# Optimization experiments

Measured on AMD Instinct MI355X. Metric: run time of the kernel, lower is better.

## Reference

```python
import jax, jax.numpy as jnp
import numpy as np

EMBED = 64
NHEADS = 8
DK = EMBED // NHEADS          # 8
PS = 32                       # patchsize[log2(8)] = (32, 32) for every head


def lrelu(z):
    return jnp.where(z > 0, z, 0.2 * z)


def conv1x1(x, w, b):
    # x: [B,C,H,W], w: [O,C], b: [O]
    return jnp.einsum('oc,bchw->bohw', w, x) + b[None, :, None, None]


def conv3x3_reflect(x, w, b, dilation=1):
    p = dilation  # pad == dilation keeps spatial size for k=3
    xp = jnp.pad(x, ((0, 0), (0, 0), (p, p), (p, p)), mode='reflect')
    y = jax.lax.conv_general_dilated(
        xp, w, window_strides=(1, 1), padding='VALID',
        rhs_dilation=(dilation, dilation),
        dimension_numbers=('NCHW', 'OIHW', 'NCHW'))
    return y + b[None, :, None, None]


def setup_inputs() -> dict:
    key = jax.random.key(0)
    ks = jax.random.split(key, 16)
    B, C, H, W = 8, EMBED, 256, 256
    g = 0.02
    inp = {
        'x': jax.random.normal(ks[0], (B, C, H, W), jnp.float32),
        'm': jax.random.uniform(ks[1], (B, 1, H, W), jnp.float32),
        'wq': jax.random.normal(ks[2], (C, C), jnp.float32) * g,
        'bq': jnp.zeros((C,), jnp.float32),
        'wk': jax.random.normal(ks[3], (C, C), jnp.float32) * g,
        'bk': jnp.zeros((C,), jnp.float32),
        'wv': jax.random.normal(ks[4], (C, C), jnp.float32) * g,
        'bv': jnp.zeros((C,), jnp.float32),
        'wo': jax.random.normal(ks[5], (C, C, 3, 3), jnp.float32) * g,
        'bo': jnp.zeros((C,), jnp.float32),
        'wf1': jax.random.normal(ks[6], (C, C, 3, 3), jnp.float32) * g,
        'bf1': jnp.zeros((C,), jnp.float32),
        'wf2': jax.random.normal(ks[7], (C, C, 3, 3), jnp.float32) * g,
        'bf2': jnp.zeros((C,), jnp.float32),
    }
    return inp


def _window(t, b, oh, ow):
    # [B, C, H, W] -> [B, nH, oh*ow, dk*ps*ps] (head = channel chunk)
    t = t.reshape(b, NHEADS, DK, oh, PS, ow, PS)
    t = t.transpose(0, 1, 3, 5, 2, 4, 6)
    return t.reshape(b, NHEADS, oh * ow, DK * PS * PS)


def _forward(x, m, wq, bq, wk, bk, wv, bv, wo, bo, wf1, bf1, wf2, bf2):
    b, c, h, w = x.shape
    oh, ow = h // PS, w // PS
    q = _window(conv1x1(x, wq, bq), b, oh, ow)
    k = _window(conv1x1(x, wk, bk), b, oh, ow)
    v = _window(conv1x1(x, wv, bv), b, oh, ow)
    # NOTE: original code calls scores.masked_fill(mm, -1e9) non-in-place and
    # discards the result, so the mask `m` does NOT affect the math. Faithful.
    scale = 1.0 / jnp.sqrt(jnp.asarray(DK * PS * PS, x.dtype))
    scores = jnp.einsum('bhqe,bhke->bhqk', q, k) * scale  # [B,nH,oh*ow,oh*ow]
    p = jax.nn.softmax(scores, axis=-1)
    y = jnp.einsum('bhqk,bhke->bhqe', p, v)
    # un-window back to [B, C, H, W] (head order == channel-chunk order)
    y = y.reshape(b, NHEADS, oh, ow, DK, PS, PS)
    y = y.transpose(0, 1, 4, 2, 5, 3, 6).reshape(b, c, h, w)
    x1 = x + lrelu(conv3x3_reflect(y, wo, bo))
    ff = lrelu(conv3x3_reflect(x1, wf1, bf1, dilation=2))
    ff = lrelu(conv3x3_reflect(ff, wf2, bf2, dilation=1))
    return x1 + ff


def reference(x, m, wq, bq, wk, bk, wv, bv, wo, bo, wf1, bf1, wf2, bf2):
    return _forward(x, m, wq, bq, wk, bk, wv, bv, wo, bo, wf1, bf1, wf2, bf2)
```

## Files before the change

kernel.cpp:

```cpp
#include <hip/hip_runtime.h>
#include <hip/hip_fp16.h>

#define SCALE 0.011048543456039806f

typedef _Float16 half8 __attribute__((ext_vector_type(8)));
typedef float f32x4 __attribute__((ext_vector_type(4)));
typedef unsigned int uint32;

__device__ inline float ldval(const float* p, int i)  { return p[i]; }
__device__ inline float ldval(const __half* p, int i) { return __half2float(p[i]); }
__device__ inline void  stval(float* p, int i, float v)  { p[i] = v; }
__device__ inline void  stval(__half* p, int i, float v) { p[i] = __float2half(v); }

__global__ __launch_bounds__(256) void prep_kernel(const float* __restrict__ wq,
                                                   const float* __restrict__ wk,
                                                   const float* __restrict__ wv,
                                                   const float* __restrict__ wo,
                                                   const float* __restrict__ wf1,
                                                   const float* __restrict__ wf2,
                                                   float* __restrict__ scr) {
    int i = blockIdx.x * 256 + threadIdx.x;
    if (i < 262144) { scr[i] = 0.f; return; }
    __half* wh = (__half*)(scr + 262144);
    int j = i - 262144;
    if (j < 12288) {
        int gm = j >> 6, c = j & 63;
        int mtx = gm >> 6, o = gm & 63;
        const float* src = (mtx == 0) ? wq : ((mtx == 1) ? wk : wv);
        wh[j] = __float2half(src[o * 64 + c]);
    } else {
        int r = j - 12288;
        int mtx = r / 36864;
        int q2 = r - mtx * 36864;
        int tap = q2 >> 12;
        int oc = q2 & 4095;
        int o = oc >> 6, c = oc & 63;
        const float* src = (mtx == 0) ? wo : ((mtx == 1) ? wf1 : wf2);
        wh[j] = __float2half(src[(o * 64 + c) * 9 + tap]);
    }
}

__global__ __launch_bounds__(512) void qkv_mfma(const float* __restrict__ x,
                                                const __half* __restrict__ wqkv,
                                                const float* __restrict__ bq,
                                                const float* __restrict__ bk,
                                                const float* __restrict__ bv,
                                                __half* __restrict__ q,
                                                __half* __restrict__ k,
                                                __half* __restrict__ v) {
    __shared__ __align__(16) __half Xs[256 * 72];
    __shared__ __align__(16) __half Ws[192 * 72];
    int t = threadIdx.x;
    int bx = blockIdx.x;
    int b = bx >> 8, row = bx & 255;
    int hw0 = row << 8;
    int bbase = b << 22;

    for (int i = 0; i < 32; i++) {
        int idx = i * 512 + t;
        int c = idx >> 8, p = idx & 255;
        Xs[p * 72 + c] = __float2half(x[bbase + (c << 16) + hw0 + p]);
    }
    const uint32* src = (const uint32*)wqkv;
    #pragma unroll
    for (int i = 0; i < 12; i++) {
        int idx = i * 512 + t;
        int o = idx >> 5, c2 = idx & 31;
        *(uint32*)&Ws[o * 72 + c2 * 2] = src[idx];
    }
    __syncthreads();

    int wave = t >> 6, lane = t & 63;
    int l15 = lane & 15, quad = lane >> 4;
    int mg = wave >> 2, ng = wave & 3;
    f32x4 acc[4][6];
    #pragma unroll
    for (int i = 0; i < 4; i++)
        #pragma unroll
        for (int m = 0; m < 6; m++) acc[i][m] = (f32x4){0.f, 0.f, 0.f, 0.f};

    #pragma unroll
    for (int kc = 0; kc < 2; kc++) {
        half8 af[6];
        #pragma unroll
        for (int m = 0; m < 6; m++)
            af[m] = *(const half8*)&Ws[((mg * 6 + m) * 16 + l15) * 72 + kc * 32 + quad * 8];
        #pragma unroll
        for (int i = 0; i < 4; i++) {
            half8 bf = *(const half8*)&Xs[(ng * 64 + i * 16 + l15) * 72 + kc * 32 + quad * 8];
            #pragma unroll
            for (int m = 0; m < 6; m++)
                acc[i][m] = __builtin_amdgcn_mfma_f32_16x16x32_f16(af[m], bf, acc[i][m], 0, 0, 0);
        }
    }
    #pragma unroll
    for (int i = 0; i < 4; i++) {
        int pix = hw0 + ng * 64 + i * 16 + l15;
        #pragma unroll
        for (int m = 0; m < 6; m++) {
            int gm = mg * 6 + m;
            int mtx = gm >> 2;
            int ob = (gm & 3) * 16 + quad * 4;
            __half* dst = (mtx == 0) ? q : ((mtx == 1) ? k : v);
            const float* bb = (mtx == 0) ? bq : ((mtx == 1) ? bk : bv);
            #pragma unroll
            for (int r = 0; r < 4; r++) {
                float z = acc[i][m][r] + bb[ob + r];
                dst[bbase + ((ob + r) << 16) + pix] = __float2half(z);
            }
        }
    }
}

__global__ __launch_bounds__(256) void scores_kernel(const __half* __restrict__ q,
                                                     const __half* __restrict__ k,
                                                     float* __restrict__ sc) {
    __shared__ float Qs[64][68];
    __shared__ float Ks[64][68];
    int ec = blockIdx.x;
    int bh = blockIdx.y;
    int b = bh >> 3, h = bh & 7;
    int cbase = ((b * 64 + h * 8 + ec) << 16);
    int t = threadIdx.x;
    int qg = t >> 4, kg = t & 15;
    float acc[4][4] = {};
    for (int j = 0; j < 16; j++) {
        __syncthreads();
        #pragma unroll
        for (int i = 0; i < 16; i++) {
            int idx = i * 256 + t;
            int wi = idx >> 6;
            int el = idx & 63;
            int eg = j * 64 + el;
            int py = eg >> 5, px = eg & 31;
            int oy = wi >> 3, ox = wi & 7;
            int a = cbase + ((oy * 32 + py) << 8) + ox * 32 + px;
            Qs[el][wi] = __half2float(q[a]);
            Ks[el][wi] = __half2float(k[a]);
        }
        __syncthreads();
        for (int e = 0; e < 64; e++) {
            float4 qv = *(const float4*)&Qs[e][qg * 4];
            float4 kv = *(const float4*)&Ks[e][kg * 4];
            float qa[4] = {qv.x, qv.y, qv.z, qv.w};
            float ka[4] = {kv.x, kv.y, kv.z, kv.w};
            #pragma unroll
            for (int i = 0; i < 4; i++)
                #pragma unroll
                for (int jj = 0; jj < 4; jj++)
                    acc[i][jj] += qa[i] * ka[jj];
        }
    }
    float* dst = sc + bh * 4096;
    #pragma unroll
    for (int i = 0; i < 4; i++)
        #pragma unroll
        for (int jj = 0; jj < 4; jj++)
            atomicAdd(&dst[(qg * 4 + i) * 64 + kg * 4 + jj], acc[i][jj]);
}

__global__ __launch_bounds__(64) void softmax_kernel(float* __restrict__ sc) {
    int row = blockIdx.x;
    int ki = threadIdx.x;
    float s = sc[row * 64 + ki] * SCALE;
    float m = s;
    #pragma unroll
    for (int off = 32; off; off >>= 1) m = fmaxf(m, __shfl_xor(m, off));
    float e = __expf(s - m);
    float sum = e;
    #pragma unroll
    for (int off = 32; off; off >>= 1) sum += __shfl_xor(sum, off);
    sc[row * 64 + ki] = e / sum;
}

__global__ __launch_bounds__(256) void attnout_kernel(const float* __restrict__ p,
                                                      const __half* __restrict__ v,
                                                      __half* __restrict__ y) {
    __shared__ float Ps[64][65];
    __shared__ float Vs[64][132];
    int dk = blockIdx.x, bh = blockIdx.y;
    int b = bh >> 3, h = bh & 7;
    int cbase = ((b * 64 + h * 8 + dk) << 16);
    int t = threadIdx.x;
    #pragma unroll
    for (int i = 0; i < 16; i++) {
        int idx = i * 256 + t;
        Ps[idx >> 6][idx & 63] = p[bh * 4096 + idx];
    }
    int qg = t >> 4, eg = t & 15;
    for (int sub = 0; sub < 8; sub++) {
        __syncthreads();
        #pragma unroll
        for (int i = 0; i < 32; i++) {
            int idx = i * 256 + t;
            int ki = idx >> 7, el = idx & 127;
            int elg = sub * 128 + el;
            int py = elg >> 5, px = elg & 31;
            int oy = ki >> 3, ox = ki & 7;
            Vs[ki][el] = __half2float(v[cbase + ((oy * 32 + py) << 8) + ox * 32 + px]);
        }
        __syncthreads();
        float acc[4][8] = {};
        for (int ki = 0; ki < 64; ki++) {
            float4 v0 = *(const float4*)&Vs[ki][eg * 8];
            float4 v1 = *(const float4*)&Vs[ki][eg * 8 + 4];
            #pragma unroll
            for (int i = 0; i < 4; i++) {
                float pv = Ps[qg * 4 + i][ki];
                acc[i][0] += pv * v0.x; acc[i][1] += pv * v0.y;
                acc[i][2] += pv * v0.z; acc[i][3] += pv * v0.w;
                acc[i][4] += pv * v1.x; acc[i][5] += pv * v1.y;
                acc[i][6] += pv * v1.z; acc[i][7] += pv * v1.w;
            }
        }
        int elg0 = sub * 128 + eg * 8;
        int py = elg0 >> 5, px = elg0 & 31;
        #pragma unroll
        for (int i = 0; i < 4; i++) {
            int wi = qg * 4 + i;
            int oy = wi >> 3, ox = wi & 7;
            int a = cbase + ((oy * 32 + py) << 8) + ox * 32 + px;
            #pragma unroll
            for (int jj = 0; jj < 8; jj++)
                y[a + jj] = __float2half(acc[i][jj]);
        }
    }
}

template <int DIL, typename TRES, typename TOUT>
__global__ __launch_bounds__(256) void conv3x3_mfma(const __half* __restrict__ in,
                                                    const __half* __restrict__ wt,
                                                    const float* __restrict__ bias,
                                                    const TRES* __restrict__ res,
                                                    TOUT* __restrict__ out) {
    constexpr int TH = 8, TW = 32;
    constexpr int PH = TH + 2 * DIL, PW = TW + 2 * DIL;
    constexpr int NP = PH * PW;
    __shared__ __align__(16) __half Xs[NP * 72];
    __shared__ __align__(16) __half Ws[64 * 72];

    int t = threadIdx.x;
    int bx = blockIdx.x;
    int tc = bx & 7, tr = (bx >> 3) & 31, b = bx >> 8;
    int x0 = tc * TW, y0 = tr * TH;
    int bbase = b << 22;

    for (int i = 0; i < NP * 64 / 256; i++) {
        int idx = i * 256 + t;
        int c = idx / NP, p = idx - c * NP;
        int py = p / PW, px = p - py * PW;
        int gy = y0 + py - DIL; gy = gy < 0 ? -gy : (gy > 255 ? 510 - gy : gy);
        int gx = x0 + px - DIL; gx = gx < 0 ? -gx : (gx > 255 ? 510 - gx : gx);
        Xs[p * 72 + c] = in[bbase + (c << 16) + (gy << 8) + gx];
    }

    int wave = t >> 6, lane = t & 63;
    int l15 = lane & 15, quad = lane >> 4;
    f32x4 acc[4][4];
    #pragma unroll
    for (int i = 0; i < 4; i++)
        #pragma unroll
        for (int m = 0; m < 4; m++) acc[i][m] = (f32x4){0.f, 0.f, 0.f, 0.f};

    for (int tap = 0; tap < 9; tap++) {
        __syncthreads();
        const uint32* src = (const uint32*)(wt + tap * 4096);
        #pragma unroll
        for (int i = 0; i < 8; i++) {
            int idx = i * 256 + t;
            int o = idx >> 5, c2 = idx & 31;
            *(uint32*)&Ws[o * 72 + c2 * 2] = src[idx];
        }
        __syncthreads();
        int ky = tap / 3, kx = tap - ky * 3;
        #pragma unroll
        for (int kc = 0; kc < 2; kc++) {
            half8 af[4];
            #pragma unroll
            for (int m = 0; m < 4; m++)
                af[m] = *(const half8*)&Ws[(m * 16 + l15) * 72 + kc * 32 + quad * 8];
            #pragma unroll
            for (int i = 0; i < 4; i++) {
                int nt = wave * 4 + i;
                int py = (nt >> 1) + ky * DIL;
                int px = (nt & 1) * 16 + l15 + kx * DIL;
                half8 bf = *(const half8*)&Xs[(py * PW + px) * 72 + kc * 32 + quad * 8];
                #pragma unroll
                for (int m = 0; m < 4; m++)
                    acc[i][m] = __builtin_amdgcn_mfma_f32_16x16x32_f16(af[m], bf, acc[i][m], 0, 0, 0);
            }
        }
    }

    #pragma unroll
    for (int i = 0; i < 4; i++) {
        int nt = wave * 4 + i;
        int hw = ((y0 + (nt >> 1)) << 8) + x0 + (nt & 1) * 16 + l15;
        #pragma unroll
        for (int m = 0; m < 4; m++) {
            #pragma unroll
            for (int r = 0; r < 4; r++) {
                int o = m * 16 + quad * 4 + r;
                float z = acc[i][m][r] + bias[o];
                z = z > 0.f ? z : 0.2f * z;
                int ga = bbase + (o << 16) + hw;
                if (res) z += ldval(res, ga);
                stval(out, ga, z);
            }
        }
    }
}

extern "C" void kernel_launch(void* const* d_in, const int* in_sizes, int n_in,
                              void* d_out, int out_size, void* d_ws, size_t ws_size,
                              hipStream_t stream) {
    const float* x   = (const float*)d_in[0];
    float*       scr = (float*)d_in[1];
    const float* wq  = (const float*)d_in[2];
    const float* bq  = (const float*)d_in[3];
    const float* wk  = (const float*)d_in[4];
    const float* bk  = (const float*)d_in[5];
    const float* wv  = (const float*)d_in[6];
    const float* bv  = (const float*)d_in[7];
    const float* wo  = (const float*)d_in[8];
    const float* bo  = (const float*)d_in[9];
    const float* wf1 = (const float*)d_in[10];
    const float* bf1 = (const float*)d_in[11];
    const float* wf2 = (const float*)d_in[12];
    const float* bf2 = (const float*)d_in[13];

    __half* wsA  = (__half*)d_ws;
    __half* wsB  = (__half*)((char*)d_ws + 67108864);
    __half* vbuf = (__half*)d_out;
    __half* ybuf = vbuf + 33554432;
    float*  outf = (float*)d_out;
    float*  sc   = scr;
    const __half* wh    = (const __half*)(scr + 262144);
    const __half* wqkv  = wh;
    const __half* wTo   = wh + 12288;
    const __half* wT1   = wh + 12288 + 36864;
    const __half* wT2   = wh + 12288 + 73728;

    prep_kernel<<<1504, 256, 0, stream>>>(wq, wk, wv, wo, wf1, wf2, scr);
    qkv_mfma<<<2048, 512, 0, stream>>>(x, wqkv, bq, bk, bv, wsA, wsB, vbuf);
    scores_kernel<<<dim3(8, 64), 256, 0, stream>>>(wsA, wsB, sc);
    softmax_kernel<<<4096, 64, 0, stream>>>(sc);
    attnout_kernel<<<dim3(8, 64), 256, 0, stream>>>(sc, vbuf, ybuf);
    conv3x3_mfma<1, float, __half><<<2048, 256, 0, stream>>>(ybuf, wTo, bo, x, wsA);
    conv3x3_mfma<2, float, __half><<<2048, 256, 0, stream>>>(wsA, wT1, bf1, (const float*)nullptr, wsB);
    conv3x3_mfma<1, __half, float><<<2048, 256, 0, stream>>>(wsB, wT2, bf2, wsA, outf);
}
```

Measured before the change: 978.1 us.

## Use NHWC intermediates, register-resident weights and swizzled LDS in 3x3 convs

Rewrites the three 3x3 conv kernels so intermediate activations between them are stored channel-last (NHWC half). Tiles can then be loaded with 16-byte vector loads instead of scalar gathers. Each wave keeps its 16 output channels' weights for all 9 taps in registers, which removes the per-tap shared-memory weight staging and 18 barriers. The input tile in LDS uses an XOR swizzle instead of padding to avoid bank conflicts. This raises register pressure (144 VGPRs for weights plus 64 accumulators), which may lower occupancy.

```diff
diff --git a/kernel.cpp b/kernel.cpp
--- a/kernel.cpp
+++ b/kernel.cpp
@@ -4,13 +4,9 @@
 #define SCALE 0.011048543456039806f
 
 typedef _Float16 half8 __attribute__((ext_vector_type(8)));
+typedef _Float16 h4    __attribute__((ext_vector_type(4)));
 typedef float f32x4 __attribute__((ext_vector_type(4)));
 typedef unsigned int uint32;
-
-__device__ inline float ldval(const float* p, int i)  { return p[i]; }
-__device__ inline float ldval(const __half* p, int i) { return __half2float(p[i]); }
-__device__ inline void  stval(float* p, int i, float v)  { p[i] = v; }
-__device__ inline void  stval(__half* p, int i, float v) { p[i] = __float2half(v); }
 
 __global__ __launch_bounds__(256) void prep_kernel(const float* __restrict__ wq,
                                                    const float* __restrict__ wk,
@@ -227,86 +223,119 @@
     }
 }
 
-template <int DIL, typename TRES, typename TOUT>
-__global__ __launch_bounds__(256) void conv3x3_mfma(const __half* __restrict__ in,
-                                                    const __half* __restrict__ wt,
-                                                    const float* __restrict__ bias,
-                                                    const TRES* __restrict__ res,
-                                                    TOUT* __restrict__ out) {
+template <int DIL, int IN_NCHW, int RES, int OUTM>
+__global__ __launch_bounds__(256) void conv3x3_v2(const _Float16* __restrict__ in,
+                                                  const _Float16* __restrict__ wt,
+                                                  const float* __restrict__ bias,
+                                                  const void* __restrict__ res,
+                                                  void* __restrict__ out) {
     constexpr int TH = 8, TW = 32;
     constexpr int PH = TH + 2 * DIL, PW = TW + 2 * DIL;
     constexpr int NP = PH * PW;
-    __shared__ __align__(16) __half Xs[NP * 72];
-    __shared__ __align__(16) __half Ws[64 * 72];
+    __shared__ __align__(16) _Float16 Xs[NP * 64];
 
     int t = threadIdx.x;
+    int wave = t >> 6, lane = t & 63;
     int bx = blockIdx.x;
     int tc = bx & 7, tr = (bx >> 3) & 31, b = bx >> 8;
     int x0 = tc * TW, y0 = tr * TH;
-    int bbase = b << 22;
-
-    for (int i = 0; i < NP * 64 / 256; i++) {
-        int idx = i * 256 + t;
-        int c = idx / NP, p = idx - c * NP;
-        int py = p / PW, px = p - py * PW;
-        int gy = y0 + py - DIL; gy = gy < 0 ? -gy : (gy > 255 ? 510 - gy : gy);
-        int gx = x0 + px - DIL; gx = gx < 0 ? -gx : (gx > 255 ? 510 - gx : gx);
-        Xs[p * 72 + c] = in[bbase + (c << 16) + (gy << 8) + gx];
-    }
-
-    int wave = t >> 6, lane = t & 63;
+    int bb = b << 22;
+
+    if (IN_NCHW) {
+        constexpr int PO = (NP + 7) / 8;
+        constexpr int SIT = (PO * 8 * 64) / 256;
+        for (int i = 0; i < SIT; i++) {
+            int s = i * 256 + t;
+            int l = s & 63, G = s >> 6;
+            int p = (G >> 3) * 8 + (l & 7);
+            int c = (G & 7) * 8 + (l >> 3);
+            int py = p / PW, px = p - py * PW;
+            int gy = y0 + py - DIL; gy = gy < 0 ? -gy : (gy > 255 ? 510 - gy : gy);
+            int gx = x0 + px - DIL; gx = gx < 0 ? -gx : (gx > 255 ? 510 - gx : gx);
+            _Float16 val = in[bb + (c << 16) + (gy << 8) + gx];
+            if (p < NP)
+                Xs[(p << 6) + (((c >> 3) ^ (p & 7)) << 3) + (c & 7)] = val;
+        }
+    } else {
+        constexpr int SLOTS = NP * 8;
+        constexpr int SIT = (SLOTS + 255) / 256;
+        half8 tmp[SIT];
+        #pragma unroll
+        for (int i = 0; i < SIT; i++) {
+            int s = i * 256 + t;
+            int p = s >> 3, c8 = s & 7;
+            int py = p / PW, px = p - py * PW;
+            int gy = y0 + py - DIL; gy = gy < 0 ? -gy : (gy > 255 ? 510 - gy : gy);
+            int gx = x0 + px - DIL; gx = gx < 0 ? -gx : (gx > 255 ? 510 - gx : gx);
+            tmp[i] = *(const half8*)(in + bb + (((gy << 8) + gx) << 6) + c8 * 8);
+        }
+        #pragma unroll
+        for (int i = 0; i < SIT; i++) {
+            int s = i * 256 + t;
+            int p = s >> 3, c8 = s & 7;
+            if (s < SLOTS)
+                *(half8*)&Xs[(p << 6) + ((c8 ^ (p & 7)) << 3)] = tmp[i];
+        }
+    }
+
     int l15 = lane & 15, quad = lane >> 4;
-    f32x4 acc[4][4];
-    #pragma unroll
-    for (int i = 0; i < 4; i++)
-        #pragma unroll
-        for (int m = 0; m < 4; m++) acc[i][m] = (f32x4){0.f, 0.f, 0.f, 0.f};
-
+    half8 af[9][2];
+    #pragma unroll
+    for (int tap = 0; tap < 9; tap++)
+        #pragma unroll
+        for (int kc = 0; kc < 2; kc++)
+            af[tap][kc] = *(const half8*)&wt[tap * 4096 + (wave * 16 + l15) * 64 + kc * 32 + quad * 8];
+
+    f32x4 acc[16];
+    #pragma unroll
+    for (int nt = 0; nt < 16; nt++) acc[nt] = (f32x4){0.f, 0.f, 0.f, 0.f};
+
+    __syncthreads();
+
+    #pragma unroll
     for (int tap = 0; tap < 9; tap++) {
-        __syncthreads();
-        const uint32* src = (const uint32*)(wt + tap * 4096);
-        #pragma unroll
-        for (int i = 0; i < 8; i++) {
-            int idx = i * 256 + t;
-            int o = idx >> 5, c2 = idx & 31;
-            *(uint32*)&Ws[o * 72 + c2 * 2] = src[idx];
-        }
-        __syncthreads();
-        int ky = tap / 3, kx = tap - ky * 3;
+        const int ky = tap / 3, kx = tap % 3;
         #pragma unroll
         for (int kc = 0; kc < 2; kc++) {
-            half8 af[4];
-            #pragma unroll
-            for (int m = 0; m < 4; m++)
-                af[m] = *(const half8*)&Ws[(m * 16 + l15) * 72 + kc * 32 + quad * 8];
-            #pragma unroll
-            for (int i = 0; i < 4; i++) {
-                int nt = wave * 4 + i;
-                int py = (nt >> 1) + ky * DIL;
-                int px = (nt & 1) * 16 + l15 + kx * DIL;
-                half8 bf = *(const half8*)&Xs[(py * PW + px) * 72 + kc * 32 + quad * 8];
-                #pragma unroll
-                for (int m = 0; m < 4; m++)
-                    acc[i][m] = __builtin_amdgcn_mfma_f32_16x16x32_f16(af[m], bf, acc[i][m], 0, 0, 0);
+            int cq = kc * 4 + quad;
+            #pragma unroll
+            for (int nt = 0; nt < 16; nt++) {
+                int p = ((nt >> 1) + ky * DIL) * PW + (nt & 1) * 16 + kx * DIL + l15;
+                half8 bf = *(const half8*)&Xs[(p << 6) + ((cq ^ (p & 7)) << 3)];
+                acc[nt] = __builtin_amdgcn_mfma_f32_16x16x32_f16(af[tap][kc], bf, acc[nt], 0, 0, 0);
             }
         }
     }
 
-    #pragma unroll
-    for (int i = 0; i < 4; i++) {
-        int nt = wave * 4 + i;
-        int hw = ((y0 + (nt >> 1)) << 8) + x0 + (nt & 1) * 16 + l15;
-        #pragma unroll
-        for (int m = 0; m < 4; m++) {
-            #pragma unroll
-            for (int r = 0; r < 4; r++) {
-                int o = m * 16 + quad * 4 + r;
-                float z = acc[i][m][r] + bias[o];
-                z = z > 0.f ? z : 0.2f * z;
-                int ga = bbase + (o << 16) + hw;
-                if (res) z += ldval(res, ga);
-                stval(out, ga, z);
-            }
+    int oc0 = wave * 16 + quad * 4;
+    f32x4 b4 = *(const f32x4*)&bias[oc0];
+    #pragma unroll
+    for (int nt = 0; nt < 16; nt++) {
+        int pixg = ((y0 + (nt >> 1)) << 8) + x0 + (nt & 1) * 16 + l15;
+        float z[4];
+        #pragma unroll
+        for (int r = 0; r < 4; r++) {
+            float w = acc[nt][r] + b4[r];
+            z[r] = w > 0.f ? w : 0.2f * w;
+        }
+        if (RES == 1) {
+            const float* rf = (const float*)res;
+            #pragma unroll
+            for (int r = 0; r < 4; r++) z[r] += rf[bb + ((oc0 + r) << 16) + pixg];
+        } else if (RES == 2) {
+            h4 rv = *(const h4*)((const _Float16*)res + bb + (pixg << 6) + oc0);
+            #pragma unroll
+            for (int r = 0; r < 4; r++) z[r] += (float)rv[r];
+        }
+        if (OUTM == 0) {
+            h4 ov;
+            #pragma unroll
+            for (int r = 0; r < 4; r++) ov[r] = (_Float16)z[r];
+            *(h4*)((_Float16*)out + bb + (pixg << 6) + oc0) = ov;
+        } else {
+            #pragma unroll
+            for (int r = 0; r < 4; r++)
+                ((float*)out)[bb + ((oc0 + r) << 16) + pixg] = z[r];
         }
     }
 }
@@ -337,16 +366,19 @@
     float*  sc   = scr;
     const __half* wh    = (const __half*)(scr + 262144);
     const __half* wqkv  = wh;
-    const __half* wTo   = wh + 12288;
-    const __half* wT1   = wh + 12288 + 36864;
-    const __half* wT2   = wh + 12288 + 73728;
+    const _Float16* wTo = (const _Float16*)(wh + 12288);
+    const _Float16* wT1 = (const _Float16*)(wh + 12288 + 36864);
+    const _Float16* wT2 = (const _Float16*)(wh + 12288 + 73728);
 
     prep_kernel<<<1504, 256, 0, stream>>>(wq, wk, wv, wo, wf1, wf2, scr);
     qkv_mfma<<<2048, 512, 0, stream>>>(x, wqkv, bq, bk, bv, wsA, wsB, vbuf);
     scores_kernel<<<dim3(8, 64), 256, 0, stream>>>(wsA, wsB, sc);
     softmax_kernel<<<4096, 64, 0, stream>>>(sc);
     attnout_kernel<<<dim3(8, 64), 256, 0, stream>>>(sc, vbuf, ybuf);
-    conv3x3_mfma<1, float, __half><<<2048, 256, 0, stream>>>(ybuf, wTo, bo, x, wsA);
-    conv3x3_mfma<2, float, __half><<<2048, 256, 0, stream>>>(wsA, wT1, bf1, (const float*)nullptr, wsB);
-    conv3x3_mfma<1, __half, float><<<2048, 256, 0, stream>>>(wsB, wT2, bf2, wsA, outf);
-}
+    conv3x3_v2<1, 1, 1, 0><<<2048, 256, 0, stream>>>((const _Float16*)ybuf, wTo, bo,
+                                                     (const void*)x, (void*)wsA);
+    conv3x3_v2<2, 0, 0, 0><<<2048, 256, 0, stream>>>((const _Float16*)wsA, wT1, bf1,
+                                                     nullptr, (void*)wsB);
+    conv3x3_v2<1, 0, 2, 1><<<2048, 256, 0, stream>>>((const _Float16*)wsB, wT2, bf2,
+                                                     (const void*)wsA, (void*)outf);
+}
```

After: 964.9 us. About the same (-1.3%).
